# Kernel optimization log

Hardware: AMD Instinct MI355X
Metric: run time of the kernel (lower is better)

## Reference

```python
import jax, jax.numpy as jnp
import numpy as np

N_NODES = 100000
N_EDGES = 1600000
IN_C, HID_C, OUT_C = 128, 64, 32


def setup_inputs() -> dict:
    key = jax.random.key(0)
    k1, k2, k3, k4 = jax.random.split(key, 4)
    x = jax.random.normal(k1, (N_NODES, IN_C), dtype=jnp.float32)
    edge_index = jax.random.randint(k2, (2, N_EDGES), 0, N_NODES, dtype=jnp.int64)
    # glorot-style init for GCN linear weights
    W1 = jax.random.normal(k3, (IN_C, HID_C), dtype=jnp.float32) * (2.0 / (IN_C + HID_C)) ** 0.5
    b1 = jnp.zeros((HID_C,), dtype=jnp.float32)
    W2 = jax.random.normal(k4, (HID_C, OUT_C), dtype=jnp.float32) * (2.0 / (HID_C + OUT_C)) ** 0.5
    b2 = jnp.zeros((OUT_C,), dtype=jnp.float32)
    return {"x": x, "edge_index": edge_index, "W1": W1, "b1": b1, "W2": W2, "b2": b2}


def _gcn_conv(h, row, col, norm, n, b):
    # gather transformed source features, scale by symmetric norm, scatter-add to targets
    msg = h[row] * norm[:, None]            # [E+N, C]
    return jax.ops.segment_sum(msg, col, num_segments=n) + b


def reference(x, edge_index, W1, b1, W2, b2):
    n = x.shape[0]
    loops = jnp.arange(n, dtype=edge_index.dtype)
    row = jnp.concatenate([edge_index[0], loops])   # sources (with self-loops)
    col = jnp.concatenate([edge_index[1], loops])   # targets
    deg = jax.ops.segment_sum(jnp.ones_like(col, dtype=x.dtype), col, num_segments=n)
    dinv = jnp.where(deg > 0, jax.lax.rsqrt(deg), 0.0)
    norm = dinv[row] * dinv[col]                    # D^{-1/2} A_hat D^{-1/2}
    h = jax.nn.relu(_gcn_conv(x @ W1, row, col, norm, n, b1))
    out = _gcn_conv(h @ W2, row, col, norm, n, b2)
    return out
```

## Files before the change

### kernel.cpp

```cpp
#include <hip/hip_runtime.h>

#define IN_C 128
#define HID_C 64
#define OUT_C 32
#define NBLK 512
#define NBUCK 512
#define CAP 5120

typedef unsigned int uint;
typedef unsigned short ushort;
typedef __attribute__((ext_vector_type(8))) short bf16x8;
typedef __attribute__((ext_vector_type(4))) float f32x4;

__device__ __forceinline__ uint bf16pair(float a, float b) {
  uint ua = __float_as_uint(a), ub = __float_as_uint(b);
  ua = (ua + 0x7FFFu + ((ua >> 16) & 1u)) >> 16;
  ub = (ub + 0x7FFFu + ((ub >> 16) & 1u)) >> 16;
  return ua | (ub << 16);
}

__device__ __forceinline__ uint bf16one(float a) {
  uint u = __float_as_uint(a);
  return (u + 0x7FFFu + ((u >> 16) & 1u)) >> 16;
}

__device__ __forceinline__ void acc8(float* acc, uint4 q) {
  acc[0] += __uint_as_float(q.x << 16);
  acc[1] += __uint_as_float(q.x & 0xFFFF0000u);
  acc[2] += __uint_as_float(q.y << 16);
  acc[3] += __uint_as_float(q.y & 0xFFFF0000u);
  acc[4] += __uint_as_float(q.z << 16);
  acc[5] += __uint_as_float(q.z & 0xFFFF0000u);
  acc[6] += __uint_as_float(q.w << 16);
  acc[7] += __uint_as_float(q.w & 0xFFFF0000u);
}


__global__ void __launch_bounds__(256) scatter_reserve_kernel(
    const int* __restrict__ row, const int* __restrict__ col,
    int* __restrict__ gcur, int* __restrict__ ebuf, int e, int epb) {
  __shared__ int hist[NBUCK];
  __shared__ int cur[NBUCK];
  int t = threadIdx.x, b = blockIdx.x;
  for (int i = t; i < NBUCK; i += 256) hist[i] = 0;
  __syncthreads();
  int s = b * epb, en = min(e, s + epb);
  for (int i = s + t; i < en; i += 256) atomicAdd(&hist[col[i] >> 8], 1);
  __syncthreads();
  for (int i = t; i < NBUCK; i += 256) {
    int h = hist[i];
    int base = h ? atomicAdd(&gcur[i], h) : 0;
    cur[i] = CAP * i + base;
  }
  __syncthreads();
  for (int i = s + t; i < en; i += 256) {
    int c = col[i], r = row[i];
    int bk = c >> 8;
    int p = atomicAdd(&cur[bk], 1);
    if (p < CAP * bk + CAP) ebuf[p] = r | ((c & 255) << 17);
  }
}

__global__ void __launch_bounds__(256) csr_kernel(const int* __restrict__ ebuf,
                                                  const int* __restrict__ gcur,
                                                  int* __restrict__ offS, int* __restrict__ offE,
                                                  int* __restrict__ srt, float* __restrict__ dinv,
                                                  int n) {
  __shared__ int cnt[256];
  __shared__ int base[256];
  int t = threadIdx.x, b = blockIdx.x;
  int es = b * CAP;
  int ec = min(gcur[b], CAP);
  cnt[t] = 0;
  __syncthreads();
  for (int i = t; i < ec; i += 256) atomicAdd(&cnt[(ebuf[es + i] >> 17) & 255], 1);
  __syncthreads();
  int v = cnt[t];
  base[t] = v;
  __syncthreads();
  for (int d = 1; d < 256; d <<= 1) {
    int a = (t >= d) ? base[t - d] : 0;
    __syncthreads();
    base[t] += a;
    __syncthreads();
  }
  int gstart = es + base[t] - v;
  int node = b * 256 + t;
  if (node < n) {
    offS[node] = gstart;
    offE[node] = gstart + v;
    dinv[node] = rsqrtf((float)(v + 1));
  }
  base[t] = gstart;
  __syncthreads();
  for (int i = t; i < ec; i += 256) {
    int pv = ebuf[es + i];
    int pos = atomicAdd(&base[(pv >> 17) & 255], 1);
    srt[pos] = pv & 0x1FFFF;
  }
}

__global__ void __launch_bounds__(256) prep_w1t_kernel(const float* __restrict__ W1,
                                                       ushort* __restrict__ w1t_hi,
                                                       ushort* __restrict__ w1t_lo) {
  int i = blockIdx.x * 256 + threadIdx.x;
  if (i < HID_C * IN_C) {
    int k = i >> 6, c = i & 63;
    float v = W1[i];
    uint h = bf16one(v);
    float lo = v - __uint_as_float(h << 16);
    w1t_hi[c * IN_C + k] = (ushort)h;
    w1t_lo[c * IN_C + k] = (ushort)bf16one(lo);
  }
}

__global__ void __launch_bounds__(256) gemm1_mfma_kernel(
    const float* __restrict__ x, const ushort* __restrict__ w1t_hi,
    const ushort* __restrict__ w1t_lo, const float* __restrict__ dinv,
    ushort* __restrict__ xw1b, int n) {
  __shared__ float eps[4][16 * 68];
  int t = threadIdx.x;
  int wv = t >> 6, lane = t & 63, m = lane & 15, q = lane >> 4;
  int row0 = blockIdx.x * 64 + wv * 16;
  int arow = min(row0 + m, n - 1);
  const float* xp = x + (size_t)arow * IN_C + q * 8;
  bf16x8 ah[4], al[4];
#pragma unroll
  for (int kb = 0; kb < 4; ++kb) {
    float4 v0 = *(const float4*)(xp + kb * 32);
    float4 v1 = *(const float4*)(xp + kb * 32 + 4);
    float vv[8] = {v0.x, v0.y, v0.z, v0.w, v1.x, v1.y, v1.z, v1.w};
    uint hu[8];
    float lf[8];
#pragma unroll
    for (int i = 0; i < 8; ++i) {
      hu[i] = bf16one(vv[i]);
      lf[i] = vv[i] - __uint_as_float(hu[i] << 16);
    }
    uint4 hq = make_uint4(hu[0] | (hu[1] << 16), hu[2] | (hu[3] << 16),
                          hu[4] | (hu[5] << 16), hu[6] | (hu[7] << 16));
    uint4 lq = make_uint4(bf16pair(lf[0], lf[1]), bf16pair(lf[2], lf[3]),
                          bf16pair(lf[4], lf[5]), bf16pair(lf[6], lf[7]));
    ah[kb] = *(bf16x8*)&hq;
    al[kb] = *(bf16x8*)&lq;
  }
  f32x4 acc[4];
#pragma unroll
  for (int ct = 0; ct < 4; ++ct) acc[ct] = (f32x4){0.f, 0.f, 0.f, 0.f};
#pragma unroll
  for (int kb = 0; kb < 4; ++kb) {
#pragma unroll
    for (int ct = 0; ct < 4; ++ct) {
      const ushort* bp = w1t_hi + (ct * 16 + m) * IN_C + kb * 32 + q * 8;
      bf16x8 bh = *(const bf16x8*)bp;
      bf16x8 bl = *(const bf16x8*)(w1t_lo + (ct * 16 + m) * IN_C + kb * 32 + q * 8);
      acc[ct] = __builtin_amdgcn_mfma_f32_16x16x32_bf16(ah[kb], bh, acc[ct], 0, 0, 0);
      acc[ct] = __builtin_amdgcn_mfma_f32_16x16x32_bf16(al[kb], bh, acc[ct], 0, 0, 0);
      acc[ct] = __builtin_amdgcn_mfma_f32_16x16x32_bf16(ah[kb], bl, acc[ct], 0, 0, 0);
    }
  }
  float* ep = eps[wv];
#pragma unroll
  for (int ct = 0; ct < 4; ++ct)
#pragma unroll
    for (int rg = 0; rg < 4; ++rg)
      ep[(q * 4 + rg) * 68 + ct * 16 + m] = acc[ct][rg];
  __syncthreads();
#pragma unroll
  for (int it = 0; it < 2; ++it) {
    int r = it * 8 + (lane >> 3), cc = lane & 7;
    int grow = row0 + r;
    if (grow < n) {
      float4 v0 = *(const float4*)&ep[r * 68 + cc * 8];
      float4 v1 = *(const float4*)&ep[r * 68 + cc * 8 + 4];
      float dv = dinv[grow];
      uint4 o = make_uint4(bf16pair(v0.x * dv, v0.y * dv), bf16pair(v0.z * dv, v0.w * dv),
                           bf16pair(v1.x * dv, v1.y * dv), bf16pair(v1.z * dv, v1.w * dv));
      *(uint4*)(xw1b + (size_t)grow * HID_C + cc * 8) = o;
    }
  }
}

__global__ void __launch_bounds__(256) gather1_gemm2_kernel(
    const int* __restrict__ offS, const int* __restrict__ offE, const int* __restrict__ srt,
    const float* __restrict__ dinv, const ushort* __restrict__ xw1b,
    const float* __restrict__ b1, const float* __restrict__ W2,
    ushort* __restrict__ hw2b, int n) {
  __shared__ float w2s[HID_C * OUT_C];
  int t = threadIdx.x;
  for (int i = t; i < HID_C * OUT_C; i += 256) w2s[i] = W2[i];
  __syncthreads();
  int g = t >> 3, fl = t & 7;
  int c = blockIdx.x * 32 + g;
  if (c >= n) return;
  int js = offS[c], je = offE[c];
  float acc[8] = {0.f, 0.f, 0.f, 0.f, 0.f, 0.f, 0.f, 0.f};
  float acc2[8] = {0.f, 0.f, 0.f, 0.f, 0.f, 0.f, 0.f, 0.f};
  int j = js;
  for (; j + 7 < je; j += 8) {
    int r0 = __builtin_nontemporal_load(srt + j);
    int r1 = __builtin_nontemporal_load(srt + j + 1);
    int r2 = __builtin_nontemporal_load(srt + j + 2);
    int r3 = __builtin_nontemporal_load(srt + j + 3);
    int r4 = __builtin_nontemporal_load(srt + j + 4);
    int r5 = __builtin_nontemporal_load(srt + j + 5);
    int r6 = __builtin_nontemporal_load(srt + j + 6);
    int r7 = __builtin_nontemporal_load(srt + j + 7);
    uint4 q0 = ((const uint4*)(xw1b + (size_t)r0 * HID_C))[fl];
    uint4 q1 = ((const uint4*)(xw1b + (size_t)r1 * HID_C))[fl];
    uint4 q2 = ((const uint4*)(xw1b + (size_t)r2 * HID_C))[fl];
    uint4 q3 = ((const uint4*)(xw1b + (size_t)r3 * HID_C))[fl];
    uint4 q4 = ((const uint4*)(xw1b + (size_t)r4 * HID_C))[fl];
    uint4 q5 = ((const uint4*)(xw1b + (size_t)r5 * HID_C))[fl];
    uint4 q6 = ((const uint4*)(xw1b + (size_t)r6 * HID_C))[fl];
    uint4 q7 = ((const uint4*)(xw1b + (size_t)r7 * HID_C))[fl];
    acc8(acc, q0); acc8(acc2, q1); acc8(acc, q2); acc8(acc2, q3);
    acc8(acc, q4); acc8(acc2, q5); acc8(acc, q6); acc8(acc2, q7);
  }
  for (; j + 3 < je; j += 4) {
    int r0 = __builtin_nontemporal_load(srt + j);
    int r1 = __builtin_nontemporal_load(srt + j + 1);
    int r2 = __builtin_nontemporal_load(srt + j + 2);
    int r3 = __builtin_nontemporal_load(srt + j + 3);
    uint4 q0 = ((const uint4*)(xw1b + (size_t)r0 * HID_C))[fl];
    uint4 q1 = ((const uint4*)(xw1b + (size_t)r1 * HID_C))[fl];
    uint4 q2 = ((const uint4*)(xw1b + (size_t)r2 * HID_C))[fl];
    uint4 q3 = ((const uint4*)(xw1b + (size_t)r3 * HID_C))[fl];
    acc8(acc, q0); acc8(acc2, q1); acc8(acc, q2); acc8(acc2, q3);
  }
  for (; j < je; ++j) {
    int r = __builtin_nontemporal_load(srt + j);
    acc8(acc, ((const uint4*)(xw1b + (size_t)r * HID_C))[fl]);
  }
  acc8(acc, ((const uint4*)(xw1b + (size_t)c * HID_C))[fl]);
  float dv = dinv[c];
  const float4* b1v = (const float4*)b1;
  float4 blo = b1v[fl * 2], bhi = b1v[fl * 2 + 1];
  float h[8];
  h[0] = (acc[0] + acc2[0]) * dv + blo.x;
  h[1] = (acc[1] + acc2[1]) * dv + blo.y;
  h[2] = (acc[2] + acc2[2]) * dv + blo.z;
  h[3] = (acc[3] + acc2[3]) * dv + blo.w;
  h[4] = (acc[4] + acc2[4]) * dv + bhi.x;
  h[5] = (acc[5] + acc2[5]) * dv + bhi.y;
  h[6] = (acc[6] + acc2[6]) * dv + bhi.z;
  h[7] = (acc[7] + acc2[7]) * dv + bhi.w;
#pragma unroll
  for (int i = 0; i < 8; ++i) h[i] = h[i] > 0.f ? h[i] : 0.f;
  int lanebase = (t & 63) & 56;
  float o0 = 0.f, o1 = 0.f, o2 = 0.f, o3 = 0.f;
#pragma unroll
  for (int s = 0; s < 8; ++s) {
    int src = lanebase | s;
#pragma unroll
    for (int i = 0; i < 8; ++i) {
      float hv = __shfl(h[i], src, 64);
      float4 w = *(const float4*)(&w2s[(s * 8 + i) * OUT_C + fl * 4]);
      o0 += hv * w.x; o1 += hv * w.y; o2 += hv * w.z; o3 += hv * w.w;
    }
  }
  float dv2 = dv;
  uint2 ov;
  ov.x = bf16pair(o0 * dv2, o1 * dv2);
  ov.y = bf16pair(o2 * dv2, o3 * dv2);
  ((uint2*)(hw2b + (size_t)c * OUT_C))[fl] = ov;
}

__global__ void __launch_bounds__(256) gather2_kernel(
    const int* __restrict__ offS, const int* __restrict__ offE, const int* __restrict__ srt,
    const float* __restrict__ dinv, const ushort* __restrict__ hw2b,
    const float* __restrict__ b2, float* __restrict__ out, int n) {
  int t = threadIdx.x;
  int g = t >> 2, fl = t & 3;
  int c = blockIdx.x * 64 + g;
  if (c >= n) return;
  int js = offS[c], je = offE[c];
  float acc[8] = {0.f, 0.f, 0.f, 0.f, 0.f, 0.f, 0.f, 0.f};
  float acc2[8] = {0.f, 0.f, 0.f, 0.f, 0.f, 0.f, 0.f, 0.f};
  int j = js;
  for (; j + 7 < je; j += 8) {
    int r0 = __builtin_nontemporal_load(srt + j);
    int r1 = __builtin_nontemporal_load(srt + j + 1);
    int r2 = __builtin_nontemporal_load(srt + j + 2);
    int r3 = __builtin_nontemporal_load(srt + j + 3);
    int r4 = __builtin_nontemporal_load(srt + j + 4);
    int r5 = __builtin_nontemporal_load(srt + j + 5);
    int r6 = __builtin_nontemporal_load(srt + j + 6);
    int r7 = __builtin_nontemporal_load(srt + j + 7);
    uint4 q0 = ((const uint4*)(hw2b + (size_t)r0 * OUT_C))[fl];
    uint4 q1 = ((const uint4*)(hw2b + (size_t)r1 * OUT_C))[fl];
    uint4 q2 = ((const uint4*)(hw2b + (size_t)r2 * OUT_C))[fl];
    uint4 q3 = ((const uint4*)(hw2b + (size_t)r3 * OUT_C))[fl];
    uint4 q4 = ((const uint4*)(hw2b + (size_t)r4 * OUT_C))[fl];
    uint4 q5 = ((const uint4*)(hw2b + (size_t)r5 * OUT_C))[fl];
    uint4 q6 = ((const uint4*)(hw2b + (size_t)r6 * OUT_C))[fl];
    uint4 q7 = ((const uint4*)(hw2b + (size_t)r7 * OUT_C))[fl];
    acc8(acc, q0); acc8(acc2, q1); acc8(acc, q2); acc8(acc2, q3);
    acc8(acc, q4); acc8(acc2, q5); acc8(acc, q6); acc8(acc2, q7);
  }
  for (; j + 3 < je; j += 4) {
    int r0 = __builtin_nontemporal_load(srt + j);
    int r1 = __builtin_nontemporal_load(srt + j + 1);
    int r2 = __builtin_nontemporal_load(srt + j + 2);
    int r3 = __builtin_nontemporal_load(srt + j + 3);
    uint4 q0 = ((const uint4*)(hw2b + (size_t)r0 * OUT_C))[fl];
    uint4 q1 = ((const uint4*)(hw2b + (size_t)r1 * OUT_C))[fl];
    uint4 q2 = ((const uint4*)(hw2b + (size_t)r2 * OUT_C))[fl];
    uint4 q3 = ((const uint4*)(hw2b + (size_t)r3 * OUT_C))[fl];
    acc8(acc, q0); acc8(acc2, q1); acc8(acc, q2); acc8(acc2, q3);
  }
  for (; j < je; ++j) {
    int r = __builtin_nontemporal_load(srt + j);
    acc8(acc, ((const uint4*)(hw2b + (size_t)r * OUT_C))[fl]);
  }
  acc8(acc, ((const uint4*)(hw2b + (size_t)c * OUT_C))[fl]);
  float dv = dinv[c];
  const float4* b2v = (const float4*)b2;
  float4 blo = b2v[fl * 2], bhi = b2v[fl * 2 + 1];
  float4 olo = {(acc[0] + acc2[0]) * dv + blo.x, (acc[1] + acc2[1]) * dv + blo.y,
                (acc[2] + acc2[2]) * dv + blo.z, (acc[3] + acc2[3]) * dv + blo.w};
  float4 ohi = {(acc[4] + acc2[4]) * dv + bhi.x, (acc[5] + acc2[5]) * dv + bhi.y,
                (acc[6] + acc2[6]) * dv + bhi.z, (acc[7] + acc2[7]) * dv + bhi.w};
  ((float4*)(out + (size_t)c * OUT_C))[fl * 2] = olo;
  ((float4*)(out + (size_t)c * OUT_C))[fl * 2 + 1] = ohi;
}

extern "C" void kernel_launch(void* const* d_in, const int* in_sizes, int n_in,
                              void* d_out, int out_size, void* d_ws, size_t ws_size,
                              hipStream_t stream) {
  const float* x  = (const float*)d_in[0];
  const int*   ei = (const int*)d_in[1];
  const float* W1 = (const float*)d_in[2];
  const float* b1 = (const float*)d_in[3];
  const float* W2 = (const float*)d_in[4];
  const float* b2 = (const float*)d_in[5];
  float* out = (float*)d_out;

  int n = in_sizes[0] / IN_C;
  int e = in_sizes[1] / 2;
  const int* row = ei;
  const int* col = ei + e;

  float* dinv = (float*)d_ws;
  int*   offS = (int*)(dinv + n);
  int*   offE = offS + n;
  int*   gcur = offE + n;
  int*   srt  = gcur + NBUCK;
  ushort* xw1b = (ushort*)(srt + (size_t)NBUCK * CAP);
  int*   ebuf = (int*)xw1b;
  ushort* hw2b = xw1b + (size_t)n * HID_C;
  ushort* w1t_hi = hw2b + (size_t)n * OUT_C;
  ushort* w1t_lo = w1t_hi + HID_C * IN_C;

  int epb = (e + NBLK - 1) / NBLK;
  int nbuckets = (n + 255) / 256;

  hipMemsetAsync(gcur, 0, NBUCK * sizeof(int), stream);
  hipLaunchKernelGGL(scatter_reserve_kernel, dim3(NBLK), dim3(256), 0, stream,
                     row, col, gcur, ebuf, e, epb);
  hipLaunchKernelGGL(csr_kernel, dim3(nbuckets), dim3(256), 0, stream,
                     ebuf, gcur, offS, offE, srt, dinv, n);
  hipLaunchKernelGGL(prep_w1t_kernel, dim3((HID_C * IN_C + 255) / 256), dim3(256), 0, stream,
                     W1, w1t_hi, w1t_lo);
  hipLaunchKernelGGL(gemm1_mfma_kernel, dim3((n + 63) / 64), dim3(256), 0, stream,
                     x, w1t_hi, w1t_lo, dinv, xw1b, n);
  hipLaunchKernelGGL(gather1_gemm2_kernel, dim3((n + 31) / 32), dim3(256), 0, stream,
                     offS, offE, srt, dinv, xw1b, b1, W2, hw2b, n);
  hipLaunchKernelGGL(gather2_kernel, dim3((n + 63) / 64), dim3(256), 0, stream,
                     offS, offE, srt, dinv, hw2b, b2, out, n);
}
```

Before: 241.4 us.

## Process nodes in degree-sorted order to balance gather work across warps

Builds a degree histogram in the CSR kernel, scans it, and constructs a permutation that orders nodes by descending in-degree (clamped at 63). Both gather kernels then process nodes through this permutation, so the thread groups in a wavefront handle nodes of similar degree and less time goes to divergent loop trip counts. The cost is two extra small kernels, the permutation indirection, and scattered rather than coalesced accesses to offS/offE/dinv and to the output rows.

```diff
diff --git a/kernel.cpp b/kernel.cpp
--- a/kernel.cpp
+++ b/kernel.cpp
@@ -6,6 +6,7 @@
 #define NBLK 512
 #define NBUCK 512
 #define CAP 5120
+#define DBIN 64
 
 typedef unsigned int uint;
 typedef unsigned short ushort;
@@ -65,13 +66,15 @@
                                                   const int* __restrict__ gcur,
                                                   int* __restrict__ offS, int* __restrict__ offE,
                                                   int* __restrict__ srt, float* __restrict__ dinv,
-                                                  int n) {
+                                                  int* __restrict__ ghist, int n) {
   __shared__ int cnt[256];
   __shared__ int base[256];
+  __shared__ int dh[DBIN];
   int t = threadIdx.x, b = blockIdx.x;
   int es = b * CAP;
   int ec = min(gcur[b], CAP);
   cnt[t] = 0;
+  if (t < DBIN) dh[t] = 0;
   __syncthreads();
   for (int i = t; i < ec; i += 256) atomicAdd(&cnt[(ebuf[es + i] >> 17) & 255], 1);
   __syncthreads();
@@ -90,6 +93,7 @@
     offS[node] = gstart;
     offE[node] = gstart + v;
     dinv[node] = rsqrtf((float)(v + 1));
+    atomicAdd(&dh[v > (DBIN - 1) ? (DBIN - 1) : v], 1);
   }
   base[t] = gstart;
   __syncthreads();
@@ -97,6 +101,43 @@
     int pv = ebuf[es + i];
     int pos = atomicAdd(&base[(pv >> 17) & 255], 1);
     srt[pos] = pv & 0x1FFFF;
+  }
+  __syncthreads();
+  if (t < DBIN && dh[t]) atomicAdd(&ghist[t], dh[t]);
+}
+
+
+__global__ void perm_scan_kernel(const int* __restrict__ ghist, int* __restrict__ gcur2) {
+  int t = threadIdx.x;
+  int s = 0;
+  for (int d = t + 1; d < DBIN; ++d) s += ghist[d];
+  gcur2[t] = s;
+}
+
+__global__ void __launch_bounds__(256) perm_build_kernel(
+    const int* __restrict__ offS, const int* __restrict__ offE,
+    int* __restrict__ gcur2, int* __restrict__ perm, int n) {
+  __shared__ int lh[DBIN];
+  __shared__ int lb[DBIN];
+  int t = threadIdx.x;
+  if (t < DBIN) lh[t] = 0;
+  __syncthreads();
+  int node = blockIdx.x * 256 + t;
+  int d = 0;
+  if (node < n) {
+    d = offE[node] - offS[node];
+    if (d > DBIN - 1) d = DBIN - 1;
+    atomicAdd(&lh[d], 1);
+  }
+  __syncthreads();
+  if (t < DBIN) {
+    int h = lh[t];
+    lb[t] = h ? atomicAdd(&gcur2[t], h) : 0;
+  }
+  __syncthreads();
+  if (node < n) {
+    int pos = atomicAdd(&lb[d], 1);
+    perm[pos] = node;
   }
 }
 
@@ -185,14 +226,15 @@
     const int* __restrict__ offS, const int* __restrict__ offE, const int* __restrict__ srt,
     const float* __restrict__ dinv, const ushort* __restrict__ xw1b,
     const float* __restrict__ b1, const float* __restrict__ W2,
-    ushort* __restrict__ hw2b, int n) {
+    const int* __restrict__ perm, ushort* __restrict__ hw2b, int n) {
   __shared__ float w2s[HID_C * OUT_C];
   int t = threadIdx.x;
   for (int i = t; i < HID_C * OUT_C; i += 256) w2s[i] = W2[i];
   __syncthreads();
   int g = t >> 3, fl = t & 7;
-  int c = blockIdx.x * 32 + g;
-  if (c >= n) return;
+  int pi = blockIdx.x * 32 + g;
+  if (pi >= n) return;
+  int c = perm[pi];
   int js = offS[c], je = offE[c];
   float acc[8] = {0.f, 0.f, 0.f, 0.f, 0.f, 0.f, 0.f, 0.f};
   float acc2[8] = {0.f, 0.f, 0.f, 0.f, 0.f, 0.f, 0.f, 0.f};
@@ -259,21 +301,22 @@
       o0 += hv * w.x; o1 += hv * w.y; o2 += hv * w.z; o3 += hv * w.w;
     }
   }
-  float dv2 = dv;
   uint2 ov;
-  ov.x = bf16pair(o0 * dv2, o1 * dv2);
-  ov.y = bf16pair(o2 * dv2, o3 * dv2);
+  ov.x = bf16pair(o0 * dv, o1 * dv);
+  ov.y = bf16pair(o2 * dv, o3 * dv);
   ((uint2*)(hw2b + (size_t)c * OUT_C))[fl] = ov;
 }
 
 __global__ void __launch_bounds__(256) gather2_kernel(
     const int* __restrict__ offS, const int* __restrict__ offE, const int* __restrict__ srt,
     const float* __restrict__ dinv, const ushort* __restrict__ hw2b,
-    const float* __restrict__ b2, float* __restrict__ out, int n) {
+    const float* __restrict__ b2, const int* __restrict__ perm,
+    float* __restrict__ out, int n) {
   int t = threadIdx.x;
   int g = t >> 2, fl = t & 3;
-  int c = blockIdx.x * 64 + g;
-  if (c >= n) return;
+  int pi = blockIdx.x * 64 + g;
+  if (pi >= n) return;
+  int c = perm[pi];
   int js = offS[c], je = offE[c];
   float acc[8] = {0.f, 0.f, 0.f, 0.f, 0.f, 0.f, 0.f, 0.f};
   float acc2[8] = {0.f, 0.f, 0.f, 0.f, 0.f, 0.f, 0.f, 0.f};
@@ -345,7 +388,10 @@
   int*   offS = (int*)(dinv + n);
   int*   offE = offS + n;
   int*   gcur = offE + n;
-  int*   srt  = gcur + NBUCK;
+  int*   ghist = gcur + NBUCK;
+  int*   gcur2 = ghist + DBIN;
+  int*   perm = gcur2 + DBIN;
+  int*   srt  = perm + n;
   ushort* xw1b = (ushort*)(srt + (size_t)NBUCK * CAP);
   int*   ebuf = (int*)xw1b;
   ushort* hw2b = xw1b + (size_t)n * HID_C;
@@ -355,17 +401,20 @@
   int epb = (e + NBLK - 1) / NBLK;
   int nbuckets = (n + 255) / 256;
 
-  hipMemsetAsync(gcur, 0, NBUCK * sizeof(int), stream);
+  hipMemsetAsync(gcur, 0, (NBUCK + DBIN) * sizeof(int), stream);
   hipLaunchKernelGGL(scatter_reserve_kernel, dim3(NBLK), dim3(256), 0, stream,
                      row, col, gcur, ebuf, e, epb);
   hipLaunchKernelGGL(csr_kernel, dim3(nbuckets), dim3(256), 0, stream,
-                     ebuf, gcur, offS, offE, srt, dinv, n);
+                     ebuf, gcur, offS, offE, srt, dinv, ghist, n);
+  hipLaunchKernelGGL(perm_scan_kernel, dim3(1), dim3(DBIN), 0, stream, ghist, gcur2);
+  hipLaunchKernelGGL(perm_build_kernel, dim3(nbuckets), dim3(256), 0, stream,
+                     offS, offE, gcur2, perm, n);
   hipLaunchKernelGGL(prep_w1t_kernel, dim3((HID_C * IN_C + 255) / 256), dim3(256), 0, stream,
                      W1, w1t_hi, w1t_lo);
   hipLaunchKernelGGL(gemm1_mfma_kernel, dim3((n + 63) / 64), dim3(256), 0, stream,
                      x, w1t_hi, w1t_lo, dinv, xw1b, n);
   hipLaunchKernelGGL(gather1_gemm2_kernel, dim3((n + 31) / 32), dim3(256), 0, stream,
-                     offS, offE, srt, dinv, xw1b, b1, W2, hw2b, n);
+                     offS, offE, srt, dinv, xw1b, b1, W2, perm, hw2b, n);
   hipLaunchKernelGGL(gather2_kernel, dim3((n + 63) / 64), dim3(256), 0, stream,
-                     offS, offE, srt, dinv, hw2b, b2, out, n);
-}
+                     offS, offE, srt, dinv, hw2b, b2, perm, out, n);
+}
```

After: 253.9 us. 1.05x slower.
